# Kernel optimization log

Measured on AMD Instinct MI355X. Metric: run time of the kernel, lower is better.

Reference implementation:

```python
import jax, jax.numpy as jnp
import numpy as np

N_POS = 8192
BATCH = 4
N_GT = 512
EPS = 1e-6
P_EXP = -1.0  # generalized-mean exponent (p < 0)


def setup_inputs() -> dict:
    key = jax.random.key(0)
    k1, k2, k3 = jax.random.split(key, 3)
    dis_matrix = jax.random.uniform(k1, (N_POS, N_POS), dtype=jnp.float32)
    prob_map = jax.random.uniform(k2, (BATCH, N_POS), dtype=jnp.float32)
    gt = jax.random.randint(k3, (BATCH, N_GT), 0, N_POS, dtype=jnp.int64 if jax.config.jax_enable_x64 else jnp.int32)
    return {"prob_map": prob_map, "gt": gt, "dis_matrix": dis_matrix}


def reference(prob_map, gt, dis_matrix):
    max_dist = jnp.max(dis_matrix)
    # global min-max normalization with detached min/range (matches torch .detach())
    pmin = jax.lax.stop_gradient(jnp.min(prob_map))
    prange = jax.lax.stop_gradient(jnp.max(prob_map) - jnp.min(prob_map))
    prob = jnp.clip((prob_map - pmin) / prange, 0.0, 1.0)  # (B, N)

    # gather gt-indexed columns: dis_matrix[:, gt] -> (N, B, G) -> (B, N, G)
    D = jnp.transpose(jnp.take(dis_matrix, gt, axis=1), (1, 0, 2))

    n_est = prob.sum(axis=1)  # (B,)
    # term 1: (1/n_est) * sum_n p_n * min_g D[n, g]
    term1 = jnp.sum(prob * jnp.min(D, axis=2), axis=1) / (n_est + EPS)  # (B,)

    # term 2: generalized mean over pixel dim of weighted distance matrix
    w = (1.0 - prob)[:, :, None] * max_dist + prob[:, :, None] * D  # (B, N, G)
    minn = jnp.mean((w + EPS) ** P_EXP, axis=1) ** (1.0 / P_EXP)  # (B, G)
    term2 = jnp.mean(minn, axis=1)  # (B,)

    return jnp.mean(term1) + jnp.mean(term2)
```

## Files before the change

### kernel.cpp

```cpp
#include <hip/hip_runtime.h>
#include <math.h>

#define N_POS 8192
#define BATCH 4
#define N_GT 512
#define BG 2048
#define EPSV 1e-6f

#define KA_BLOCKS 1024
#define ROWS_A 8
#define KC_BLOCKS 1024
#define ROWS_C 8
#define RG 32
#define CHUNKS_PER_RG (KC_BLOCKS / RG)

#define WS_DPACK 0
#define WS_PARTS (N_POS * BG)
#define WS_PARTS2 (WS_PARTS + KC_BLOCKS * BG)
#define WS_MIND  (WS_PARTS2 + RG * BG)
#define WS_MAXP  (WS_MIND + BATCH * N_POS)
#define WS_SC    (WS_MAXP + KA_BLOCKS)

typedef __attribute__((ext_vector_type(4))) float f32x4;

__global__ __launch_bounds__(256) void whd_kA(const float* __restrict__ dis,
                                              const int* __restrict__ gt,
                                              float* __restrict__ wsf) {
    __shared__ float rowbuf[N_POS];
    __shared__ unsigned short gtl[BG];
    __shared__ float smax[4];
    const int t = threadIdx.x;
    const int wv = t >> 6, lane = t & 63;
    const int row0 = blockIdx.x * ROWS_A;
    float* dpack = wsf + WS_DPACK;
    float* minD = wsf + WS_MIND;

    for (int i = t; i < BG; i += 256) gtl[i] = (unsigned short)gt[i];

    f32x4 pre[8];
    {
        const f32x4* src = (const f32x4*)(dis + (size_t)row0 * N_POS);
        #pragma unroll
        for (int j = 0; j < 8; j++) pre[j] = __builtin_nontemporal_load(src + t + 256 * j);
    }
    __syncthreads();
    int c[8];
    #pragma unroll
    for (int k = 0; k < 8; k++) c[k] = gtl[8 * t + k];

    float tmax = -INFINITY;
    for (int r = 0; r < ROWS_A; r++) {
        const int n = row0 + r;
        f32x4* dstl = (f32x4*)rowbuf;
        #pragma unroll
        for (int j = 0; j < 8; j++) {
            f32x4 v = pre[j];
            tmax = fmaxf(tmax, fmaxf(fmaxf(v.x, v.y), fmaxf(v.z, v.w)));
            dstl[t + 256 * j] = v;
        }
        if (r + 1 < ROWS_A) {
            const f32x4* srcn = (const f32x4*)(dis + (size_t)(n + 1) * N_POS);
            #pragma unroll
            for (int j = 0; j < 8; j++) pre[j] = __builtin_nontemporal_load(srcn + t + 256 * j);
        }
        __syncthreads();
        float g0 = rowbuf[c[0]], g1 = rowbuf[c[1]], g2 = rowbuf[c[2]], g3 = rowbuf[c[3]];
        float g4 = rowbuf[c[4]], g5 = rowbuf[c[5]], g6 = rowbuf[c[6]], g7 = rowbuf[c[7]];
        f32x4* dst = (f32x4*)(dpack + (size_t)n * BG + 8 * t);
        f32x4 pk0; pk0.x = g0; pk0.y = g1; pk0.z = g2; pk0.w = g3;
        f32x4 pk1; pk1.x = g4; pk1.y = g5; pk1.z = g6; pk1.w = g7;
        dst[0] = pk0;
        dst[1] = pk1;
        float m = fminf(fminf(fminf(g0, g1), fminf(g2, g3)),
                        fminf(fminf(g4, g5), fminf(g6, g7)));
        #pragma unroll
        for (int off = 32; off; off >>= 1) m = fminf(m, __shfl_xor(m, off, 64));
        if (lane == 0) minD[wv * N_POS + n] = m;
        if (r + 1 < ROWS_A) __syncthreads();
    }
    #pragma unroll
    for (int off = 32; off; off >>= 1) tmax = fmaxf(tmax, __shfl_down(tmax, off, 64));
    if (lane == 0) smax[wv] = tmax;
    __syncthreads();
    if (t == 0)
        wsf[WS_MAXP + blockIdx.x] = fmaxf(fmaxf(smax[0], smax[1]), fmaxf(smax[2], smax[3]));
}

__global__ __launch_bounds__(1024) void whd_kB(const float* __restrict__ prob,
                                               float* __restrict__ wsf) {
    __shared__ float sA[16], sB[16], sC[16];
    const int t = threadIdx.x, wv = t >> 6, lane = t & 63;

    float m = -INFINITY;
    for (int i = t; i < KA_BLOCKS; i += 1024) m = fmaxf(m, wsf[WS_MAXP + i]);
    #pragma unroll
    for (int off = 32; off; off >>= 1) m = fmaxf(m, __shfl_xor(m, off, 64));

    float lmin = INFINITY, lmax = -INFINITY;
    const f32x4* p4 = (const f32x4*)prob;
    for (int i = t; i < BATCH * N_POS / 4; i += 1024) {
        f32x4 v = p4[i];
        lmin = fminf(fminf(lmin, fminf(v.x, v.y)), fminf(v.z, v.w));
        lmax = fmaxf(fmaxf(lmax, fmaxf(v.x, v.y)), fmaxf(v.z, v.w));
    }
    #pragma unroll
    for (int off = 32; off; off >>= 1) {
        lmin = fminf(lmin, __shfl_xor(lmin, off, 64));
        lmax = fmaxf(lmax, __shfl_xor(lmax, off, 64));
    }
    if (lane == 0) { sA[wv] = m; sB[wv] = lmin; sC[wv] = lmax; }
    __syncthreads();
    if (t == 0) {
        float maxd = -INFINITY, mn = INFINITY, mx = -INFINITY;
        #pragma unroll
        for (int i = 0; i < 16; i++) {
            maxd = fmaxf(maxd, sA[i]); mn = fminf(mn, sB[i]); mx = fmaxf(mx, sC[i]);
        }
        wsf[WS_SC + 0] = maxd;
        wsf[WS_SC + 1] = mn;
        wsf[WS_SC + 2] = mx - mn;
        wsf[WS_SC + 11] = 0.f;
        wsf[WS_SC + 12] = 0.f;
        sB[0] = mn; sC[0] = 1.0f / (mx - mn);
    }
    __syncthreads();
    const float pmin = sB[0], invr = sC[0];

    const f32x4* d4 = (const f32x4*)(wsf + WS_MIND);
    for (int b = 0; b < BATCH; b++) {
        float sp = 0.f, spm = 0.f;
        for (int i = t; i < N_POS / 4; i += 1024) {
            f32x4 v = p4[b * (N_POS / 4) + i];
            f32x4 dm = d4[b * (N_POS / 4) + i];
            float p;
            p = fminf(fmaxf((v.x - pmin) * invr, 0.f), 1.f); sp += p; spm += p * dm.x;
            p = fminf(fmaxf((v.y - pmin) * invr, 0.f), 1.f); sp += p; spm += p * dm.y;
            p = fminf(fmaxf((v.z - pmin) * invr, 0.f), 1.f); sp += p; spm += p * dm.z;
            p = fminf(fmaxf((v.w - pmin) * invr, 0.f), 1.f); sp += p; spm += p * dm.w;
        }
        #pragma unroll
        for (int off = 32; off; off >>= 1) {
            sp += __shfl_xor(sp, off, 64);
            spm += __shfl_xor(spm, off, 64);
        }
        __syncthreads();
        if (lane == 0) { sA[wv] = sp; sB[wv] = spm; }
        __syncthreads();
        if (t == 0) {
            float a = 0.f, c2 = 0.f;
            #pragma unroll
            for (int i = 0; i < 16; i++) { a += sA[i]; c2 += sB[i]; }
            wsf[WS_SC + 3 + b] = a;
            wsf[WS_SC + 7 + b] = c2;
        }
    }
}

__global__ __launch_bounds__(256) void whd_kC(const float* __restrict__ prob,
                                              float* __restrict__ wsf) {
    const int t = threadIdx.x;
    const int wv = t >> 6;
    const int row0 = blockIdx.x * ROWS_C;
    const float* dpack = wsf + WS_DPACK;
    const float maxd = wsf[WS_SC + 0];
    const float pmin = wsf[WS_SC + 1];
    const float invr = 1.0f / wsf[WS_SC + 2];
    float acc[8];
    #pragma unroll
    for (int k = 0; k < 8; k++) acc[k] = 0.f;
    #pragma unroll
    for (int r = 0; r < ROWS_C; r++) {
        const int n = row0 + r;
        float p = (prob[wv * N_POS + n] - pmin) * invr;
        p = fminf(fmaxf(p, 0.f), 1.f);
        const f32x4* rp = (const f32x4*)(dpack + (size_t)n * BG + 8 * t);
        f32x4 v0 = __builtin_nontemporal_load(rp);
        f32x4 v1 = __builtin_nontemporal_load(rp + 1);
        acc[0] += 1.0f / (fmaf(p, v0.x - maxd, maxd) + EPSV);
        acc[1] += 1.0f / (fmaf(p, v0.y - maxd, maxd) + EPSV);
        acc[2] += 1.0f / (fmaf(p, v0.z - maxd, maxd) + EPSV);
        acc[3] += 1.0f / (fmaf(p, v0.w - maxd, maxd) + EPSV);
        acc[4] += 1.0f / (fmaf(p, v1.x - maxd, maxd) + EPSV);
        acc[5] += 1.0f / (fmaf(p, v1.y - maxd, maxd) + EPSV);
        acc[6] += 1.0f / (fmaf(p, v1.z - maxd, maxd) + EPSV);
        acc[7] += 1.0f / (fmaf(p, v1.w - maxd, maxd) + EPSV);
    }
    f32x4* op = (f32x4*)(wsf + WS_PARTS + (size_t)blockIdx.x * BG + 8 * t);
    f32x4 o0; o0.x = acc[0]; o0.y = acc[1]; o0.z = acc[2]; o0.w = acc[3];
    f32x4 o1; o1.x = acc[4]; o1.y = acc[5]; o1.z = acc[6]; o1.w = acc[7];
    op[0] = o0;
    op[1] = o1;
}

__global__ __launch_bounds__(256) void whd_kD1(float* __restrict__ wsf) {
    const int t = threadIdx.x;
    const int col = blockIdx.x * 256 + t;
    const int rg = blockIdx.y;
    const float* parts = wsf + WS_PARTS + (size_t)rg * CHUNKS_PER_RG * BG;
    float s = 0.f;
    #pragma unroll 8
    for (int ch = 0; ch < CHUNKS_PER_RG; ch++) s += parts[(size_t)ch * BG + col];
    wsf[WS_PARTS2 + (size_t)rg * BG + col] = s;
}

__global__ __launch_bounds__(256) void whd_kD2(float* __restrict__ wsf,
                                               float* __restrict__ out) {
    __shared__ float red[4];
    const int t = threadIdx.x;
    const int col = blockIdx.x * 256 + t;
    const float* p2 = wsf + WS_PARTS2;
    float s = 0.f;
    #pragma unroll
    for (int rg = 0; rg < RG; rg++) s += p2[(size_t)rg * BG + col];
    float val = (float)N_POS / s;
    #pragma unroll
    for (int off = 32; off; off >>= 1) val += __shfl_xor(val, off, 64);
    if ((t & 63) == 0) red[t >> 6] = val;
    __syncthreads();
    if (t == 0) {
        float blocksum = red[0] + red[1] + red[2] + red[3];
        atomicAdd(&wsf[WS_SC + 11], blocksum);
        __threadfence();
        unsigned prev = atomicAdd((unsigned*)(wsf + WS_SC + 12), 1u);
        if (prev == gridDim.x - 1) {
            float t2sum = atomicAdd(&wsf[WS_SC + 11], 0.0f);
            float term1 = 0.f;
            #pragma unroll
            for (int b = 0; b < BATCH; b++)
                term1 += wsf[WS_SC + 7 + b] / (wsf[WS_SC + 3 + b] + EPSV);
            out[0] = term1 * (1.0f / BATCH) + t2sum * (1.0f / BG);
        }
    }
}

extern "C" void kernel_launch(void* const* d_in, const int* in_sizes, int n_in,
                              void* d_out, int out_size, void* d_ws, size_t ws_size,
                              hipStream_t stream) {
    const float* prob = (const float*)d_in[0];
    const int* gt = (const int*)d_in[1];
    const float* dis = (const float*)d_in[2];
    float* out = (float*)d_out;
    float* wsf = (float*)d_ws;

    whd_kA<<<KA_BLOCKS, 256, 0, stream>>>(dis, gt, wsf);
    whd_kB<<<1, 1024, 0, stream>>>(prob, wsf);
    whd_kC<<<KC_BLOCKS, 256, 0, stream>>>(prob, wsf);
    whd_kD1<<<dim3(BG / 256, RG), 256, 0, stream>>>(wsf);
    whd_kD2<<<BG / 256, 256, 0, stream>>>(wsf, out);
}
```

Baseline: 398.9 us.

## Fuse column reduction into kC via atomics and last-block finalize

Drops the two partial-sum reduction kernels (kD1, kD2). kC now adds its per-column accumulators directly into a small global column buffer with float atomics, and the last block to finish, found through a ticket counter, computes the final reciprocal means and writes the output. kC also uses half as many blocks, each handling 16 rows, so there are fewer atomics per column. The change removes two launches and the partial-sum buffer traffic, at the cost of atomic contention on 2048 addresses and a nondeterministic float summation order.

Result: slower. 491.2 us (+23.1%).

```diff
diff --git a/kernel.cpp b/kernel.cpp
--- a/kernel.cpp
+++ b/kernel.cpp
@@ -9,15 +9,12 @@
 
 #define KA_BLOCKS 1024
 #define ROWS_A 8
-#define KC_BLOCKS 1024
-#define ROWS_C 8
-#define RG 32
-#define CHUNKS_PER_RG (KC_BLOCKS / RG)
+#define KC_BLOCKS 512
+#define ROWS_C 16
 
 #define WS_DPACK 0
-#define WS_PARTS (N_POS * BG)
-#define WS_PARTS2 (WS_PARTS + KC_BLOCKS * BG)
-#define WS_MIND  (WS_PARTS2 + RG * BG)
+#define WS_COLS  (N_POS * BG)
+#define WS_MIND  (WS_COLS + BG)
 #define WS_MAXP  (WS_MIND + BATCH * N_POS)
 #define WS_SC    (WS_MAXP + KA_BLOCKS)
 
@@ -91,6 +88,8 @@
     __shared__ float sA[16], sB[16], sC[16];
     const int t = threadIdx.x, wv = t >> 6, lane = t & 63;
 
+    for (int i = t; i < BG; i += 1024) wsf[WS_COLS + i] = 0.f;
+
     float m = -INFINITY;
     for (int i = t; i < KA_BLOCKS; i += 1024) m = fmaxf(m, wsf[WS_MAXP + i]);
     #pragma unroll
@@ -119,7 +118,6 @@
         wsf[WS_SC + 0] = maxd;
         wsf[WS_SC + 1] = mn;
         wsf[WS_SC + 2] = mx - mn;
-        wsf[WS_SC + 11] = 0.f;
         wsf[WS_SC + 12] = 0.f;
         sB[0] = mn; sC[0] = 1.0f / (mx - mn);
     }
@@ -157,18 +155,23 @@
 }
 
 __global__ __launch_bounds__(256) void whd_kC(const float* __restrict__ prob,
-                                              float* __restrict__ wsf) {
+                                              float* __restrict__ wsf,
+                                              float* __restrict__ out) {
+    __shared__ int sflag;
+    __shared__ float red[4];
     const int t = threadIdx.x;
     const int wv = t >> 6;
+    const int lane = t & 63;
     const int row0 = blockIdx.x * ROWS_C;
     const float* dpack = wsf + WS_DPACK;
+    float* cols = wsf + WS_COLS;
     const float maxd = wsf[WS_SC + 0];
     const float pmin = wsf[WS_SC + 1];
     const float invr = 1.0f / wsf[WS_SC + 2];
     float acc[8];
     #pragma unroll
     for (int k = 0; k < 8; k++) acc[k] = 0.f;
-    #pragma unroll
+    #pragma unroll 8
     for (int r = 0; r < ROWS_C; r++) {
         const int n = row0 + r;
         float p = (prob[wv * N_POS + n] - pmin) * invr;
@@ -185,45 +188,29 @@
         acc[6] += 1.0f / (fmaf(p, v1.z - maxd, maxd) + EPSV);
         acc[7] += 1.0f / (fmaf(p, v1.w - maxd, maxd) + EPSV);
     }
-    f32x4* op = (f32x4*)(wsf + WS_PARTS + (size_t)blockIdx.x * BG + 8 * t);
-    f32x4 o0; o0.x = acc[0]; o0.y = acc[1]; o0.z = acc[2]; o0.w = acc[3];
-    f32x4 o1; o1.x = acc[4]; o1.y = acc[5]; o1.z = acc[6]; o1.w = acc[7];
-    op[0] = o0;
-    op[1] = o1;
-}
-
-__global__ __launch_bounds__(256) void whd_kD1(float* __restrict__ wsf) {
-    const int t = threadIdx.x;
-    const int col = blockIdx.x * 256 + t;
-    const int rg = blockIdx.y;
-    const float* parts = wsf + WS_PARTS + (size_t)rg * CHUNKS_PER_RG * BG;
-    float s = 0.f;
-    #pragma unroll 8
-    for (int ch = 0; ch < CHUNKS_PER_RG; ch++) s += parts[(size_t)ch * BG + col];
-    wsf[WS_PARTS2 + (size_t)rg * BG + col] = s;
-}
-
-__global__ __launch_bounds__(256) void whd_kD2(float* __restrict__ wsf,
-                                               float* __restrict__ out) {
-    __shared__ float red[4];
-    const int t = threadIdx.x;
-    const int col = blockIdx.x * 256 + t;
-    const float* p2 = wsf + WS_PARTS2;
-    float s = 0.f;
-    #pragma unroll
-    for (int rg = 0; rg < RG; rg++) s += p2[(size_t)rg * BG + col];
-    float val = (float)N_POS / s;
-    #pragma unroll
-    for (int off = 32; off; off >>= 1) val += __shfl_xor(val, off, 64);
-    if ((t & 63) == 0) red[t >> 6] = val;
+    #pragma unroll
+    for (int k = 0; k < 8; k++) atomicAdd(&cols[8 * t + k], acc[k]);
+    __threadfence();
     __syncthreads();
     if (t == 0) {
-        float blocksum = red[0] + red[1] + red[2] + red[3];
-        atomicAdd(&wsf[WS_SC + 11], blocksum);
+        unsigned prev = atomicAdd((unsigned*)(wsf + WS_SC + 12), 1u);
+        sflag = (prev == (unsigned)(KC_BLOCKS - 1)) ? 1 : 0;
+    }
+    __syncthreads();
+    if (sflag) {
         __threadfence();
-        unsigned prev = atomicAdd((unsigned*)(wsf + WS_SC + 12), 1u);
-        if (prev == gridDim.x - 1) {
-            float t2sum = atomicAdd(&wsf[WS_SC + 11], 0.0f);
+        float vsum = 0.f;
+        #pragma unroll
+        for (int k = 0; k < 8; k++) {
+            float s = atomicAdd(&cols[8 * t + k], 0.0f);
+            vsum += (float)N_POS / s;
+        }
+        #pragma unroll
+        for (int off = 32; off; off >>= 1) vsum += __shfl_xor(vsum, off, 64);
+        if (lane == 0) red[wv] = vsum;
+        __syncthreads();
+        if (t == 0) {
+            float t2sum = red[0] + red[1] + red[2] + red[3];
             float term1 = 0.f;
             #pragma unroll
             for (int b = 0; b < BATCH; b++)
@@ -244,7 +231,5 @@
 
     whd_kA<<<KA_BLOCKS, 256, 0, stream>>>(dis, gt, wsf);
     whd_kB<<<1, 1024, 0, stream>>>(prob, wsf);
-    whd_kC<<<KC_BLOCKS, 256, 0, stream>>>(prob, wsf);
-    whd_kD1<<<dim3(BG / 256, RG), 256, 0, stream>>>(wsf);
-    whd_kD2<<<BG / 256, 256, 0, stream>>>(wsf, out);
-}
+    whd_kC<<<KC_BLOCKS, 256, 0, stream>>>(prob, wsf, out);
+}
```
